# Kernel optimization log

Measured on AMD Instinct MI355X. Metric: run time of the kernel, lower is better.

The kernel has to match this reference:

```python
import jax, jax.numpy as jnp
import numpy as np

B, A, C = 128, 8732, 21

def setup_inputs() -> dict:
    key = jax.random.key(0)
    k1, k2, k3, k4 = jax.random.split(key, 4)
    return {
        "location_output": jax.random.normal(k1, (B, A, 4), dtype=jnp.float32),
        "classifi_output": jax.random.normal(k2, (B, A, C), dtype=jnp.float32),
        "location_label": jax.random.normal(k3, (B, A, 4), dtype=jnp.float32),
        "classifi_label": jax.random.randint(k4, (B, A), 0, C, dtype=jnp.int64),
    }

def reference(location_output, classifi_output, location_label, classifi_label):
    mask = classifi_label > 0                      # [B, A] positive anchors
    pos_num = mask.sum(axis=1)                     # [B]

    # SmoothL1 (beta=1), summed over the 4 box coords, masked to positives
    diff = location_output - location_label
    ad = jnp.abs(diff)
    sl1 = jnp.where(ad < 1.0, 0.5 * diff * diff, ad - 0.5).sum(axis=-1)  # [B, A]
    loc_loss = (sl1 * mask.astype(sl1.dtype)).sum(axis=-1)               # [B]

    # Per-anchor cross entropy
    logp = jax.nn.log_softmax(classifi_output, axis=-1)                  # [B, A, C]
    con = -jnp.take_along_axis(logp, classifi_label[..., None], axis=-1)[..., 0]  # [B, A]

    # Hard negative mining: rank negatives by CE (descending), keep top 3*pos_num
    con_neg = jnp.where(mask, 0.0, con)
    rank = jnp.argsort(jnp.argsort(-con_neg, axis=1), axis=1)            # rank in descending order
    neg_num = jnp.minimum(3 * pos_num, A)
    neg_num = jnp.where(neg_num == 0, 3, neg_num)
    neg_mask = rank < neg_num[:, None]

    con_loss = (con * (mask.astype(con.dtype) + neg_mask.astype(con.dtype))).sum(axis=1)  # [B]

    total = loc_loss + con_loss
    denom = jnp.where(pos_num != 0, pos_num, 1).astype(total.dtype)
    return (total / denom).mean()
```

## Files before the change

### kernel.cpp

```cpp
#include <hip/hip_runtime.h>

#define NBATCH 128
#define NANCH  8732
#define NCLS   21
#define GRPS   2183
#define SUBS   9


__device__ __forceinline__ float waveReduceF(float v) {
    #pragma unroll
    for (int o = 32; o > 0; o >>= 1) v += __shfl_down(v, o, 64);
    return v;
}
__device__ __forceinline__ unsigned waveReduceU(unsigned v) {
    #pragma unroll
    for (int o = 32; o > 0; o >>= 1) v += __shfl_down(v, o, 64);
    return v;
}

__device__ __forceinline__ float con_from_row(const float* __restrict__ row, int lbl) {
    float m = row[0];
    #pragma unroll
    for (int c = 1; c < NCLS; ++c) m = fmaxf(m, row[c]);
    float s = 0.f;
    #pragma unroll
    for (int c = 0; c < NCLS; ++c) s += __expf(row[c] - m);
    return m + __logf(s) - row[lbl];
}

__global__ __launch_bounds__(256, 3) void anchor_kernel(
    const float*  __restrict__ loc_out,
    const float*  __restrict__ cls_out,
    const float*  __restrict__ loc_lab,
    const int*    __restrict__ labels,
    float4* __restrict__ partial)
{
    const int b   = blockIdx.y;
    const int s   = blockIdx.x;
    const int tid = threadIdx.x;
    const int g   = s * 256 + tid;

    float loc_s = 0.f, all_s = 0.f, pos_s = 0.f;
    unsigned pc = 0;

    if (g < GRPS) {
        const size_t ba0 = (size_t)b * NANCH + (size_t)g * 4;

        const int4 lbl4 = *(const int4*)(labels + ba0);
        const float4* __restrict__ cp = (const float4*)(cls_out + ba0 * NCLS);
        float f[84];
        #pragma unroll
        for (int i = 0; i < 21; ++i) {
            const float4 v = cp[i];
            f[4*i+0] = v.x; f[4*i+1] = v.y; f[4*i+2] = v.z; f[4*i+3] = v.w;
        }
        float4 lo[4], ll[4];
        #pragma unroll
        for (int j = 0; j < 4; ++j) {
            lo[j] = ((const float4*)loc_out)[ba0 + j];
            ll[j] = ((const float4*)loc_lab)[ba0 + j];
        }
        int lbls[4] = { lbl4.x, lbl4.y, lbl4.z, lbl4.w };

        #pragma unroll
        for (int j = 0; j < 4; ++j) {
            const int lbl = lbls[j];
            float m   = f[21*j];
            float tgt = f[21*j];
            #pragma unroll
            for (int cc = 1; cc < NCLS; ++cc) {
                const float v = f[21*j + cc];
                m = fmaxf(m, v);
                tgt = (cc == lbl) ? v : tgt;
            }
            float sum = 0.f;
            #pragma unroll
            for (int cc = 0; cc < NCLS; ++cc)
                sum += __expf(f[21*j + cc] - m);

            const float con = m + __logf(sum) - tgt;
            all_s += con;
            if (lbl > 0) {
                pos_s += con;
                pc++;
                const float d0 = lo[j].x - ll[j].x, d1 = lo[j].y - ll[j].y,
                            d2 = lo[j].z - ll[j].z, d3 = lo[j].w - ll[j].w;
                const float a0 = fabsf(d0), a1 = fabsf(d1),
                            a2 = fabsf(d2), a3 = fabsf(d3);
                loc_s += ((a0 < 1.f) ? 0.5f * d0 * d0 : (a0 - 0.5f))
                       + ((a1 < 1.f) ? 0.5f * d1 * d1 : (a1 - 0.5f))
                       + ((a2 < 1.f) ? 0.5f * d2 * d2 : (a2 - 0.5f))
                       + ((a3 < 1.f) ? 0.5f * d3 * d3 : (a3 - 0.5f));
            }
        }
    }

    loc_s = waveReduceF(loc_s);
    all_s = waveReduceF(all_s);
    pos_s = waveReduceF(pos_s);
    pc    = waveReduceU(pc);

    __shared__ float sL[4], sA[4], sP[4];
    __shared__ unsigned sC[4];
    const int w = tid >> 6, lane = tid & 63;
    if (lane == 0) { sL[w] = loc_s; sA[w] = all_s; sP[w] = pos_s; sC[w] = pc; }
    __syncthreads();
    if (tid == 0) {
        float L = sL[0] + sL[1] + sL[2] + sL[3];
        float S = sA[0] + sA[1] + sA[2] + sA[3];
        float P = sP[0] + sP[1] + sP[2] + sP[3];
        unsigned C = sC[0] + sC[1] + sC[2] + sC[3];
        partial[b * SUBS + s] = make_float4(L, S, P, (float)C);
    }
}

__global__ __launch_bounds__(256) void finalize_kernel(
    const float* __restrict__ cls_out,
    const int*   __restrict__ labels,
    const float4* __restrict__ partial,
    float* __restrict__ out)
{
    const int tid = threadIdx.x;

    __shared__ float sLoc[NBATCH], sPos[NBATCH], sCnt[NBATCH], sConl[NBATCH];
    __shared__ unsigned sK[NBATCH];
    __shared__ unsigned nflag;
    if (tid == 0) nflag = 0;
    __syncthreads();

    if (tid < NBATCH) {
        float loc = 0.f, all = 0.f, pos = 0.f, cnt = 0.f;
        #pragma unroll
        for (int c = 0; c < SUBS; ++c) {
            float4 p = partial[tid * SUBS + c];
            loc += p.x; all += p.y; pos += p.z; cnt += p.w;
        }
        unsigned k = 3u * (unsigned)cnt;
        if (k > NANCH) k = NANCH;
        if (k == 0u) k = 3u;
        sLoc[tid] = loc; sPos[tid] = pos; sCnt[tid] = cnt;
        sConl[tid] = all + pos;
        if (k < NANCH) { sK[tid] = k; atomicAdd(&nflag, 1u); }
        else sK[tid] = 0u;
    }
    __syncthreads();

    if (nflag) {
        __shared__ float    rF[256];
        __shared__ unsigned rU[256];
        for (int b2 = 0; b2 < NBATCH; ++b2) {
            unsigned k = sK[b2];
            if (!k) continue;

            auto count_gt = [&](float t) -> unsigned {
                unsigned cc = 0;
                for (int an = tid; an < NANCH; an += 256) {
                    size_t ba = (size_t)b2 * NANCH + an;
                    int lbl = labels[ba];
                    if (lbl > 0) continue;
                    float con = con_from_row(cls_out + ba * NCLS, lbl);
                    if (con > t) cc++;
                }
                rU[tid] = cc; __syncthreads();
                for (int o = 128; o > 0; o >>= 1) {
                    if (tid < o) rU[tid] += rU[tid + o];
                    __syncthreads();
                }
                unsigned r = rU[0]; __syncthreads();
                return r;
            };

            unsigned cpos = count_gt(0.0f);
            float negpart = 0.f;

            if (k <= cpos) {
                unsigned lo = 0u, hi = 0x7F800000u;
                while (hi - lo > 1u) {
                    unsigned mid = lo + (hi - lo) / 2u;
                    unsigned cc = count_gt(__uint_as_float(mid));
                    if (cc >= k) lo = mid; else hi = mid;
                }
                float v = __uint_as_float(hi);
                float ss = 0.f; unsigned c1 = 0;
                for (int an = tid; an < NANCH; an += 256) {
                    size_t ba = (size_t)b2 * NANCH + an;
                    int lbl = labels[ba];
                    if (lbl > 0) continue;
                    float con = con_from_row(cls_out + ba * NCLS, lbl);
                    if (con > v) { ss += con; c1++; }
                }
                rF[tid] = ss; rU[tid] = c1; __syncthreads();
                for (int o = 128; o > 0; o >>= 1) {
                    if (tid < o) { rF[tid] += rF[tid + o]; rU[tid] += rU[tid + o]; }
                    __syncthreads();
                }
                negpart = rF[0] + (float)(k - rU[0]) * v;
                __syncthreads();
            } else {
                if (tid == 0) {
                    float np = 0.f;
                    unsigned mrem = k - cpos;
                    for (int an = 0; an < NANCH; ++an) {
                        size_t ba = (size_t)b2 * NANCH + an;
                        int lbl = labels[ba];
                        float con = con_from_row(cls_out + ba * NCLS, lbl);
                        float cneg = (lbl > 0) ? 0.f : con;
                        if (cneg > 0.f) np += con;
                        else if (mrem > 0u) { np += con; mrem--; }
                    }
                    rF[0] = np;
                }
                __syncthreads();
                negpart = rF[0];
                __syncthreads();
            }

            if (tid == 0) sConl[b2] = sPos[b2] + negpart;
            __syncthreads();
        }
    }

    float t = 0.f;
    if (tid < NBATCH) {
        float denom = (sCnt[tid] != 0.f) ? sCnt[tid] : 1.f;
        t = (sLoc[tid] + sConl[tid]) / denom;
    }
    t = waveReduceF(t);
    __shared__ float sW[4];
    const int w = tid >> 6, lane = tid & 63;
    if (lane == 0) sW[w] = t;
    __syncthreads();
    if (tid == 0) out[0] = (sW[0] + sW[1] + sW[2] + sW[3]) * (1.f / NBATCH);
}

extern "C" void kernel_launch(void* const* d_in, const int* in_sizes, int n_in,
                              void* d_out, int out_size, void* d_ws, size_t ws_size,
                              hipStream_t stream) {
    const float* loc_out = (const float*)d_in[0];
    const float* cls_out = (const float*)d_in[1];
    const float* loc_lab = (const float*)d_in[2];
    const int*   labels  = (const int*)d_in[3];
    float* out = (float*)d_out;
    float4* partial = (float4*)d_ws;

    dim3 grid(SUBS, NBATCH);
    anchor_kernel<<<grid, 256, 0, stream>>>(loc_out, cls_out, loc_lab, labels, partial);
    finalize_kernel<<<1, 256, 0, stream>>>(cls_out, labels, partial, out);
}
```

Measured before the change: 177.8 us.

## Process one anchor per thread with strided double-buffered loads

Each thread now handles about five anchors spaced by a grid-wide stride instead of four contiguous anchors. The loads use two ping-pong buffers so the next anchor's loads are in flight while the current one is computed. Each thread's 21-float row read is no longer contiguous across the wave, which changes the coalescing pattern. Fewer registers per thread allow occupancy hint 4 and a grid of 8 blocks per batch.

Measured after the change: 176.3 us. Within noise of the previous version (-0.8%).

```diff
diff --git a/kernel.cpp b/kernel.cpp
--- a/kernel.cpp
+++ b/kernel.cpp
@@ -3,8 +3,8 @@
 #define NBATCH 128
 #define NANCH  8732
 #define NCLS   21
-#define GRPS   2183
-#define SUBS   9
+#define SUBSX  8
+#define STEP   (SUBSX * 256)
 
 
 __device__ __forceinline__ float waveReduceF(float v) {
@@ -28,7 +28,81 @@
     return m + __logf(s) - row[lbl];
 }
 
-__global__ __launch_bounds__(256, 3) void anchor_kernel(
+struct Abuf {
+    float4 r0, r1, r2, r3, r4;
+    float  r5;
+    float4 lo, ll;
+    int    lbl;
+};
+
+__device__ __forceinline__ void load_anchor(
+    Abuf& bf, const float* __restrict__ cls_out,
+    const float4* __restrict__ loc_out, const float4* __restrict__ loc_lab,
+    const int* __restrict__ labels, size_t ba, bool valid)
+{
+    if (valid) {
+        const float* __restrict__ row = cls_out + ba * NCLS;
+        bf.lbl = labels[ba];
+        bf.r0 = *(const float4*)(row +  0);
+        bf.r1 = *(const float4*)(row +  4);
+        bf.r2 = *(const float4*)(row +  8);
+        bf.r3 = *(const float4*)(row + 12);
+        bf.r4 = *(const float4*)(row + 16);
+        bf.r5 = row[20];
+        bf.lo = loc_out[ba];
+        bf.ll = loc_lab[ba];
+    } else {
+        bf.lbl = 0;
+    }
+}
+
+__device__ __forceinline__ void compute_anchor(
+    const Abuf& bf, bool valid,
+    float& loc_s, float& all_s, float& pos_s, unsigned& pc)
+{
+    if (!valid) return;
+    const int lbl = bf.lbl;
+    float m   = bf.r0.x;
+    float tgt = bf.r0.x;
+    #define MAXSEL(i, comp) { const float v_ = (comp); m = fmaxf(m, v_); \
+                              tgt = (lbl == (i)) ? v_ : tgt; }
+    MAXSEL( 1, bf.r0.y) MAXSEL( 2, bf.r0.z) MAXSEL( 3, bf.r0.w)
+    MAXSEL( 4, bf.r1.x) MAXSEL( 5, bf.r1.y) MAXSEL( 6, bf.r1.z) MAXSEL( 7, bf.r1.w)
+    MAXSEL( 8, bf.r2.x) MAXSEL( 9, bf.r2.y) MAXSEL(10, bf.r2.z) MAXSEL(11, bf.r2.w)
+    MAXSEL(12, bf.r3.x) MAXSEL(13, bf.r3.y) MAXSEL(14, bf.r3.z) MAXSEL(15, bf.r3.w)
+    MAXSEL(16, bf.r4.x) MAXSEL(17, bf.r4.y) MAXSEL(18, bf.r4.z) MAXSEL(19, bf.r4.w)
+    MAXSEL(20, bf.r5)
+    #undef MAXSEL
+
+    float sum = __expf(bf.r0.x - m) + __expf(bf.r0.y - m)
+              + __expf(bf.r0.z - m) + __expf(bf.r0.w - m)
+              + __expf(bf.r1.x - m) + __expf(bf.r1.y - m)
+              + __expf(bf.r1.z - m) + __expf(bf.r1.w - m)
+              + __expf(bf.r2.x - m) + __expf(bf.r2.y - m)
+              + __expf(bf.r2.z - m) + __expf(bf.r2.w - m)
+              + __expf(bf.r3.x - m) + __expf(bf.r3.y - m)
+              + __expf(bf.r3.z - m) + __expf(bf.r3.w - m)
+              + __expf(bf.r4.x - m) + __expf(bf.r4.y - m)
+              + __expf(bf.r4.z - m) + __expf(bf.r4.w - m)
+              + __expf(bf.r5 - m);
+
+    const float con = m + __logf(sum) - tgt;
+    all_s += con;
+    if (lbl > 0) {
+        pos_s += con;
+        pc++;
+        const float d0 = bf.lo.x - bf.ll.x, d1 = bf.lo.y - bf.ll.y,
+                    d2 = bf.lo.z - bf.ll.z, d3 = bf.lo.w - bf.ll.w;
+        const float a0 = fabsf(d0), a1 = fabsf(d1),
+                    a2 = fabsf(d2), a3 = fabsf(d3);
+        loc_s += ((a0 < 1.f) ? 0.5f * d0 * d0 : (a0 - 0.5f))
+               + ((a1 < 1.f) ? 0.5f * d1 * d1 : (a1 - 0.5f))
+               + ((a2 < 1.f) ? 0.5f * d2 * d2 : (a2 - 0.5f))
+               + ((a3 < 1.f) ? 0.5f * d3 * d3 : (a3 - 0.5f));
+    }
+}
+
+__global__ __launch_bounds__(256, 4) void anchor_kernel(
     const float*  __restrict__ loc_out,
     const float*  __restrict__ cls_out,
     const float*  __restrict__ loc_lab,
@@ -38,62 +112,28 @@
     const int b   = blockIdx.y;
     const int s   = blockIdx.x;
     const int tid = threadIdx.x;
-    const int g   = s * 256 + tid;
+    const int a0  = s * 256 + tid;
+    const size_t base = (size_t)b * NANCH;
+
+    const float4* lo_p = (const float4*)loc_out;
+    const float4* ll_p = (const float4*)loc_lab;
 
     float loc_s = 0.f, all_s = 0.f, pos_s = 0.f;
     unsigned pc = 0;
 
-    if (g < GRPS) {
-        const size_t ba0 = (size_t)b * NANCH + (size_t)g * 4;
-
-        const int4 lbl4 = *(const int4*)(labels + ba0);
-        const float4* __restrict__ cp = (const float4*)(cls_out + ba0 * NCLS);
-        float f[84];
-        #pragma unroll
-        for (int i = 0; i < 21; ++i) {
-            const float4 v = cp[i];
-            f[4*i+0] = v.x; f[4*i+1] = v.y; f[4*i+2] = v.z; f[4*i+3] = v.w;
-        }
-        float4 lo[4], ll[4];
-        #pragma unroll
-        for (int j = 0; j < 4; ++j) {
-            lo[j] = ((const float4*)loc_out)[ba0 + j];
-            ll[j] = ((const float4*)loc_lab)[ba0 + j];
-        }
-        int lbls[4] = { lbl4.x, lbl4.y, lbl4.z, lbl4.w };
-
-        #pragma unroll
-        for (int j = 0; j < 4; ++j) {
-            const int lbl = lbls[j];
-            float m   = f[21*j];
-            float tgt = f[21*j];
-            #pragma unroll
-            for (int cc = 1; cc < NCLS; ++cc) {
-                const float v = f[21*j + cc];
-                m = fmaxf(m, v);
-                tgt = (cc == lbl) ? v : tgt;
-            }
-            float sum = 0.f;
-            #pragma unroll
-            for (int cc = 0; cc < NCLS; ++cc)
-                sum += __expf(f[21*j + cc] - m);
-
-            const float con = m + __logf(sum) - tgt;
-            all_s += con;
-            if (lbl > 0) {
-                pos_s += con;
-                pc++;
-                const float d0 = lo[j].x - ll[j].x, d1 = lo[j].y - ll[j].y,
-                            d2 = lo[j].z - ll[j].z, d3 = lo[j].w - ll[j].w;
-                const float a0 = fabsf(d0), a1 = fabsf(d1),
-                            a2 = fabsf(d2), a3 = fabsf(d3);
-                loc_s += ((a0 < 1.f) ? 0.5f * d0 * d0 : (a0 - 0.5f))
-                       + ((a1 < 1.f) ? 0.5f * d1 * d1 : (a1 - 0.5f))
-                       + ((a2 < 1.f) ? 0.5f * d2 * d2 : (a2 - 0.5f))
-                       + ((a3 < 1.f) ? 0.5f * d3 * d3 : (a3 - 0.5f));
-            }
-        }
-    }
+    Abuf A, B;
+    const bool v4 = a0 < (NANCH - 4 * STEP);
+
+    load_anchor(A, cls_out, lo_p, ll_p, labels, base + a0,            true);
+    load_anchor(B, cls_out, lo_p, ll_p, labels, base + a0 + 1 * STEP, true);
+    compute_anchor(A, true, loc_s, all_s, pos_s, pc);
+    load_anchor(A, cls_out, lo_p, ll_p, labels, base + a0 + 2 * STEP, true);
+    compute_anchor(B, true, loc_s, all_s, pos_s, pc);
+    load_anchor(B, cls_out, lo_p, ll_p, labels, base + a0 + 3 * STEP, true);
+    compute_anchor(A, true, loc_s, all_s, pos_s, pc);
+    load_anchor(A, cls_out, lo_p, ll_p, labels, base + a0 + 4 * STEP, v4);
+    compute_anchor(B, true, loc_s, all_s, pos_s, pc);
+    compute_anchor(A, v4,   loc_s, all_s, pos_s, pc);
 
     loc_s = waveReduceF(loc_s);
     all_s = waveReduceF(all_s);
@@ -110,7 +150,7 @@
         float S = sA[0] + sA[1] + sA[2] + sA[3];
         float P = sP[0] + sP[1] + sP[2] + sP[3];
         unsigned C = sC[0] + sC[1] + sC[2] + sC[3];
-        partial[b * SUBS + s] = make_float4(L, S, P, (float)C);
+        partial[b * SUBSX + s] = make_float4(L, S, P, (float)C);
     }
 }
 
@@ -131,8 +171,8 @@
     if (tid < NBATCH) {
         float loc = 0.f, all = 0.f, pos = 0.f, cnt = 0.f;
         #pragma unroll
-        for (int c = 0; c < SUBS; ++c) {
-            float4 p = partial[tid * SUBS + c];
+        for (int c = 0; c < SUBSX; ++c) {
+            float4 p = partial[tid * SUBSX + c];
             loc += p.x; all += p.y; pos += p.z; cnt += p.w;
         }
         unsigned k = 3u * (unsigned)cnt;
@@ -243,7 +283,7 @@
     float* out = (float*)d_out;
     float4* partial = (float4*)d_ws;
 
-    dim3 grid(SUBS, NBATCH);
+    dim3 grid(SUBSX, NBATCH);
     anchor_kernel<<<grid, 256, 0, stream>>>(loc_out, cls_out, loc_lab, labels, partial);
     finalize_kernel<<<1, 256, 0, stream>>>(cls_out, labels, partial, out);
 }
```

## Stage class logits through LDS with async global_load_lds triple buffering

Applied to the files above, without the earlier changes.

Restructures the anchor kernel so each block covers five strided rounds of 256 anchors, staging logits and labels into a triple-buffered LDS ring with direct global-to-LDS loads and explicit vmcnt waits. Each thread then computes one anchor's cross entropy from LDS. Localization data is read only for positive anchors. The aim is to overlap memory latency with compute and keep loads coalesced, at the cost of more LDS per block (occupancy bound lowered to 2), hand-tuned wait counts and clamped tail loads.

Result: no change. 177.1 us (-0.4%).

```diff
diff --git a/kernel.cpp b/kernel.cpp
--- a/kernel.cpp
+++ b/kernel.cpp
@@ -3,8 +3,12 @@
 #define NBATCH 128
 #define NANCH  8732
 #define NCLS   21
-#define GRPS   2183
-#define SUBS   9
+#define SUBSX  8
+#define STEP   2048
+#define F4CLS  1344
+#define F4ALL  1408
+#define CLS_F4_MAX ((size_t)NBATCH * NANCH * NCLS / 4 - 1)
+#define LAB_F4_MAX ((size_t)NBATCH * NANCH / 4 - 1)
 
 
 __device__ __forceinline__ float waveReduceF(float v) {
@@ -28,70 +32,124 @@
     return m + __logf(s) - row[lbl];
 }
 
-__global__ __launch_bounds__(256, 3) void anchor_kernel(
+__device__ __forceinline__ void gload_lds16(const float4* g, float4* l) {
+    __builtin_amdgcn_global_load_lds(
+        (const __attribute__((address_space(1))) void*)g,
+        (__attribute__((address_space(3))) void*)l,
+        16, 0, 0);
+}
+
+#define WAIT_PAIR(lo, hi)                                            \
+    do {                                                             \
+        if (wid < 2) asm volatile("s_waitcnt vmcnt(" #lo ")" ::: "memory"); \
+        else         asm volatile("s_waitcnt vmcnt(" #hi ")" ::: "memory"); \
+        __builtin_amdgcn_sched_barrier(0);                           \
+    } while (0)
+
+__global__ __launch_bounds__(256, 2) void anchor_kernel(
     const float*  __restrict__ loc_out,
     const float*  __restrict__ cls_out,
     const float*  __restrict__ loc_lab,
     const int*    __restrict__ labels,
     float4* __restrict__ partial)
 {
+    __shared__ float4 buf[3][F4ALL];
+
     const int b   = blockIdx.y;
     const int s   = blockIdx.x;
     const int tid = threadIdx.x;
-    const int g   = s * 256 + tid;
-
-    float loc_s = 0.f, all_s = 0.f, pos_s = 0.f;
+    const int wid = tid >> 6, lane = tid & 63;
+
+    const size_t ba_blk = (size_t)b * NANCH + s * 256;
+    const float4* cls4 = (const float4*)cls_out;
+    const float4* lab4 = (const float4*)labels;
+
+    const int wstart = (wid == 0) ? 0 : (wid == 1) ? 320 : (wid == 2) ? 640 : 1024;
+    const int wcnt   = (wid < 2) ? 5 : 6;
+
+    auto stage = [&](float4* bufp, int r) {
+        const size_t ba0     = ba_blk + (size_t)r * STEP;
+        const size_t cls_f4b = ba0 * NCLS / 4;
+        const size_t lab_f4b = ba0 / 4;
+        for (int i = 0; i < wcnt; ++i) {
+            const int uidx = wstart + i * 64;
+            const int idx  = uidx + lane;
+            const float4* src;
+            if (uidx < F4CLS) {
+                size_t g = cls_f4b + idx;
+                if (g > CLS_F4_MAX) g = CLS_F4_MAX;
+                src = cls4 + g;
+            } else {
+                size_t g = lab_f4b + (idx - F4CLS);
+                if (g > LAB_F4_MAX) g = LAB_F4_MAX;
+                src = lab4 + g;
+            }
+            gload_lds16(src, bufp + uidx);
+        }
+    };
+
+    float all_s = 0.f, pos_s = 0.f, loc_s = 0.f;
     unsigned pc = 0;
 
-    if (g < GRPS) {
-        const size_t ba0 = (size_t)b * NANCH + (size_t)g * 4;
-
-        const int4 lbl4 = *(const int4*)(labels + ba0);
-        const float4* __restrict__ cp = (const float4*)(cls_out + ba0 * NCLS);
-        float f[84];
+    auto compute_ce = [&](const float4* bufp, bool valid) -> int {
+        if (!valid) return 0;
+        const float* buff = (const float*)bufp;
+        const int lbl = ((const int*)buff)[F4CLS * 4 + tid];
+        const float* row = buff + tid * NCLS;
+        float m = row[0];
         #pragma unroll
-        for (int i = 0; i < 21; ++i) {
-            const float4 v = cp[i];
-            f[4*i+0] = v.x; f[4*i+1] = v.y; f[4*i+2] = v.z; f[4*i+3] = v.w;
-        }
-        float4 lo[4], ll[4];
+        for (int c = 1; c < NCLS; ++c) m = fmaxf(m, row[c]);
+        float sum = 0.f;
         #pragma unroll
-        for (int j = 0; j < 4; ++j) {
-            lo[j] = ((const float4*)loc_out)[ba0 + j];
-            ll[j] = ((const float4*)loc_lab)[ba0 + j];
-        }
-        int lbls[4] = { lbl4.x, lbl4.y, lbl4.z, lbl4.w };
-
-        #pragma unroll
-        for (int j = 0; j < 4; ++j) {
-            const int lbl = lbls[j];
-            float m   = f[21*j];
-            float tgt = f[21*j];
-            #pragma unroll
-            for (int cc = 1; cc < NCLS; ++cc) {
-                const float v = f[21*j + cc];
-                m = fmaxf(m, v);
-                tgt = (cc == lbl) ? v : tgt;
-            }
-            float sum = 0.f;
-            #pragma unroll
-            for (int cc = 0; cc < NCLS; ++cc)
-                sum += __expf(f[21*j + cc] - m);
-
-            const float con = m + __logf(sum) - tgt;
-            all_s += con;
-            if (lbl > 0) {
-                pos_s += con;
-                pc++;
-                const float d0 = lo[j].x - ll[j].x, d1 = lo[j].y - ll[j].y,
-                            d2 = lo[j].z - ll[j].z, d3 = lo[j].w - ll[j].w;
-                const float a0 = fabsf(d0), a1 = fabsf(d1),
-                            a2 = fabsf(d2), a3 = fabsf(d3);
-                loc_s += ((a0 < 1.f) ? 0.5f * d0 * d0 : (a0 - 0.5f))
-                       + ((a1 < 1.f) ? 0.5f * d1 * d1 : (a1 - 0.5f))
-                       + ((a2 < 1.f) ? 0.5f * d2 * d2 : (a2 - 0.5f))
-                       + ((a3 < 1.f) ? 0.5f * d3 * d3 : (a3 - 0.5f));
-            }
+        for (int c = 0; c < NCLS; ++c) sum += __expf(row[c] - m);
+        const float tgt = row[lbl];
+        const float con = m + __logf(sum) - tgt;
+        all_s += con;
+        if (lbl > 0) { pos_s += con; pc++; }
+        return lbl;
+    };
+
+    const bool v4 = (s * 256 + tid + 4 * STEP) < NANCH;
+    int lblA[5];
+
+    stage(buf[0], 0);
+    stage(buf[1], 1);
+    stage(buf[2], 2);
+
+    WAIT_PAIR(10, 12);
+    __builtin_amdgcn_s_barrier();
+    lblA[0] = compute_ce(buf[0], true);
+    __builtin_amdgcn_s_barrier();
+    stage(buf[0], 3);
+    WAIT_PAIR(10, 12);
+    __builtin_amdgcn_s_barrier();
+    lblA[1] = compute_ce(buf[1], true);
+    __builtin_amdgcn_s_barrier();
+    stage(buf[1], 4);
+    WAIT_PAIR(10, 12);
+    __builtin_amdgcn_s_barrier();
+    lblA[2] = compute_ce(buf[2], true);
+    WAIT_PAIR(5, 6);
+    __builtin_amdgcn_s_barrier();
+    lblA[3] = compute_ce(buf[0], true);
+    WAIT_PAIR(0, 0);
+    __builtin_amdgcn_s_barrier();
+    lblA[4] = compute_ce(buf[1], v4);
+
+    #pragma unroll
+    for (int r = 0; r < 5; ++r) {
+        if (lblA[r] > 0) {
+            const size_t ba = ba_blk + (size_t)r * STEP + tid;
+            const float4 lo4 = ((const float4*)loc_out)[ba];
+            const float4 ll4 = ((const float4*)loc_lab)[ba];
+            const float d0 = lo4.x - ll4.x, d1 = lo4.y - ll4.y,
+                        d2 = lo4.z - ll4.z, d3 = lo4.w - ll4.w;
+            const float a0 = fabsf(d0), a1 = fabsf(d1),
+                        a2 = fabsf(d2), a3 = fabsf(d3);
+            loc_s += ((a0 < 1.f) ? 0.5f * d0 * d0 : (a0 - 0.5f))
+                   + ((a1 < 1.f) ? 0.5f * d1 * d1 : (a1 - 0.5f))
+                   + ((a2 < 1.f) ? 0.5f * d2 * d2 : (a2 - 0.5f))
+                   + ((a3 < 1.f) ? 0.5f * d3 * d3 : (a3 - 0.5f));
         }
     }
 
@@ -102,15 +160,14 @@
 
     __shared__ float sL[4], sA[4], sP[4];
     __shared__ unsigned sC[4];
-    const int w = tid >> 6, lane = tid & 63;
-    if (lane == 0) { sL[w] = loc_s; sA[w] = all_s; sP[w] = pos_s; sC[w] = pc; }
+    if (lane == 0) { sL[wid] = loc_s; sA[wid] = all_s; sP[wid] = pos_s; sC[wid] = pc; }
     __syncthreads();
     if (tid == 0) {
         float L = sL[0] + sL[1] + sL[2] + sL[3];
         float S = sA[0] + sA[1] + sA[2] + sA[3];
         float P = sP[0] + sP[1] + sP[2] + sP[3];
         unsigned C = sC[0] + sC[1] + sC[2] + sC[3];
-        partial[b * SUBS + s] = make_float4(L, S, P, (float)C);
+        partial[b * SUBSX + s] = make_float4(L, S, P, (float)C);
     }
 }
 
@@ -131,8 +188,8 @@
     if (tid < NBATCH) {
         float loc = 0.f, all = 0.f, pos = 0.f, cnt = 0.f;
         #pragma unroll
-        for (int c = 0; c < SUBS; ++c) {
-            float4 p = partial[tid * SUBS + c];
+        for (int c = 0; c < SUBSX; ++c) {
+            float4 p = partial[tid * SUBSX + c];
             loc += p.x; all += p.y; pos += p.z; cnt += p.w;
         }
         unsigned k = 3u * (unsigned)cnt;
@@ -243,7 +300,7 @@
     float* out = (float*)d_out;
     float4* partial = (float4*)d_ws;
 
-    dim3 grid(SUBS, NBATCH);
+    dim3 grid(SUBSX, NBATCH);
     anchor_kernel<<<grid, 256, 0, stream>>>(loc_out, cls_out, loc_lab, labels, partial);
     finalize_kernel<<<1, 256, 0, stream>>>(cls_out, labels, partial, out);
 }
```
